# Kernel optimization log

Hardware: AMD Instinct MI355X
Metric: run time of the kernel (lower is better)

Reference implementation:

```python
import jax, jax.numpy as jnp
import numpy as np

EMBED_DIM = 256
NUM_HEADS = 8
PROJ_DIM = EMBED_DIM // NUM_HEADS


def setup_inputs() -> dict:
    key = jax.random.key(0)
    ks = jax.random.split(key, 5)
    scale = 1.0 / np.sqrt(EMBED_DIM)
    inputs = jax.random.normal(ks[0], (2, 12, 12, 12, EMBED_DIM), dtype=jnp.float32)
    Wq = jax.random.normal(ks[1], (EMBED_DIM, EMBED_DIM), dtype=jnp.float32) * scale
    Wk = jax.random.normal(ks[2], (EMBED_DIM, EMBED_DIM), dtype=jnp.float32) * scale
    Wv = jax.random.normal(ks[3], (EMBED_DIM, EMBED_DIM), dtype=jnp.float32) * scale
    Wo = jax.random.normal(ks[4], (EMBED_DIM, EMBED_DIM), dtype=jnp.float32) * scale
    z = jnp.zeros((EMBED_DIM,), dtype=jnp.float32)
    return {"inputs": inputs, "Wq": Wq, "bq": z, "Wk": Wk, "bk": z,
            "Wv": Wv, "bv": z, "Wo": Wo, "bo": z}


def reference(inputs, Wq, bq, Wk, bk, Wv, bv, Wo, bo):
    B, h, w, d, E = inputs.shape
    S = h * w * d  # flattened spatial sequence
    x = inputs.reshape(B, S, E)
    # projections + head split: [B, S, E] -> [B, H, S, P]
    def split_heads(t):
        return t.reshape(B, S, NUM_HEADS, PROJ_DIM).transpose(0, 2, 1, 3)
    q = split_heads(x @ Wq + bq)
    k = split_heads(x @ Wk + bk)
    v = split_heads(x @ Wv + bv)
    # NOTE: original module does NOT scale by 1/sqrt(proj_dim)
    scores = jnp.einsum('bhsp,bhtp->bhst', q, k)  # [B, H, S, S]
    attn = jax.nn.softmax(scores, axis=-1)
    out = jnp.einsum('bhst,bhtp->bhsp', attn, v)  # [B, H, S, P]
    out = out.transpose(0, 2, 1, 3).reshape(B, h, w, d, E)
    return out @ Wo + bo
```

## Files before the change

kernel.cpp:

```cpp
#include <hip/hip_runtime.h>
#include <math.h>

#define EMBED 256
#define HEADS 8
#define PDIM  32
#define BATCH 2
#define SEQ   1728
#define NTOK  (BATCH*SEQ)
#define NE    (NTOK*EMBED)
#define LOG2E 1.44269504088896f

typedef __attribute__((ext_vector_type(8))) __bf16 bf16x8;
typedef __attribute__((ext_vector_type(4))) float  f32x4;
typedef unsigned short ushort_t;

static __device__ __forceinline__ unsigned short f2bf_rne(float f) {
    union { float f; unsigned u; } x; x.f = f;
    unsigned r = x.u + 0x7fffu + ((x.u >> 16) & 1u);
    return (unsigned short)(r >> 16);
}
static __device__ __forceinline__ float bf2f(unsigned short h) {
    union { unsigned u; float f; } x; x.u = ((unsigned)h) << 16;
    return x.f;
}

__global__ __launch_bounds__(256) void convert_x_kernel(
    const float* __restrict__ x, ushort_t* __restrict__ xhi, ushort_t* __restrict__ xlo)
{
    const int i = (blockIdx.x * 256 + threadIdx.x) * 4;
    const float4 v = *(const float4*)&x[i];
    ushort4 h, l;
    h.x = f2bf_rne(v.x); l.x = f2bf_rne(v.x - bf2f(h.x));
    h.y = f2bf_rne(v.y); l.y = f2bf_rne(v.y - bf2f(h.y));
    h.z = f2bf_rne(v.z); l.z = f2bf_rne(v.z - bf2f(h.z));
    h.w = f2bf_rne(v.w); l.w = f2bf_rne(v.w - bf2f(h.w));
    *(ushort4*)&xhi[i] = h;
    *(ushort4*)&xlo[i] = l;
}

__global__ __launch_bounds__(256) void convert_w_kernel(
    const float* __restrict__ Wq, const float* __restrict__ Wk,
    const float* __restrict__ Wv, const float* __restrict__ Wo,
    ushort_t* __restrict__ wthi, ushort_t* __restrict__ wtlo)
{
    const int mat = blockIdx.z;
    const float* __restrict__ W = (mat == 0) ? Wq : (mat == 1) ? Wk : (mat == 2) ? Wv : Wo;
    const int k0 = blockIdx.x * 64, n0 = blockIdx.y * 64;
    const int t = threadIdx.x;

    __shared__ float Ws[64][68];
    {
        const int rr = t >> 4, cc = (t & 15) << 2;
        #pragma unroll
        for (int rep = 0; rep < 4; ++rep) {
            const int row = rr + rep * 16;
            *(float4*)&Ws[row][cc] = *(const float4*)&W[(size_t)(k0 + row) * EMBED + n0 + cc];
        }
    }
    __syncthreads();

    const int nl = t & 63;
    const int kc = (t >> 6) << 4;
    ushort_t hv[16], lv[16];
    #pragma unroll
    for (int kk = 0; kk < 16; ++kk) {
        const float v = Ws[kc + kk][nl];
        hv[kk] = f2bf_rne(v);
        lv[kk] = f2bf_rne(v - bf2f(hv[kk]));
    }
    ushort_t* dh = wthi + (size_t)mat * 65536 + (size_t)(n0 + nl) * EMBED + k0 + kc;
    ushort_t* dl = wtlo + (size_t)mat * 65536 + (size_t)(n0 + nl) * EMBED + k0 + kc;
    #pragma unroll
    for (int c = 0; c < 4; ++c) {
        *(ushort4*)&dh[c * 4] = *(ushort4*)&hv[c * 4];
        *(ushort4*)&dl[c * 4] = *(ushort4*)&lv[c * 4];
    }
}

__global__ __launch_bounds__(64) void qkv_gemm_kernel(
    const ushort_t* __restrict__ xhi, const ushort_t* __restrict__ xlo,
    const ushort_t* __restrict__ wthi, const ushort_t* __restrict__ wtlo,
    const float* __restrict__ bq, const float* __restrict__ bk, const float* __restrict__ bv,
    ushort_t* __restrict__ qo, ushort_t* __restrict__ ko, ushort_t* __restrict__ vt)
{
    const int lane = threadIdx.x, li = lane & 15, quad = lane >> 4;
    const int m0 = blockIdx.x * 64, n0 = blockIdx.y * 32, z = blockIdx.z;

    const ushort_t* aph = xhi + (size_t)(m0 + li) * EMBED + quad * 8;
    const ushort_t* apl = xlo + (size_t)(m0 + li) * EMBED + quad * 8;
    const ushort_t* bph = wthi + (size_t)z * 65536 + (size_t)(n0 + li) * EMBED + quad * 8;
    const ushort_t* bpl = wtlo + (size_t)z * 65536 + (size_t)(n0 + li) * EMBED + quad * 8;

    f32x4 acc[4][2];
    #pragma unroll
    for (int mt = 0; mt < 4; ++mt)
        #pragma unroll
        for (int nt = 0; nt < 2; ++nt)
            acc[mt][nt] = (f32x4){0.f, 0.f, 0.f, 0.f};

    #pragma unroll 2
    for (int k0 = 0; k0 < EMBED; k0 += 32) {
        bf16x8 ah[4], al[4], bh[2], bl[2];
        #pragma unroll
        for (int mt = 0; mt < 4; ++mt) {
            ah[mt] = *(const bf16x8*)(aph + (size_t)mt * 16 * EMBED + k0);
            al[mt] = *(const bf16x8*)(apl + (size_t)mt * 16 * EMBED + k0);
        }
        #pragma unroll
        for (int nt = 0; nt < 2; ++nt) {
            bh[nt] = *(const bf16x8*)(bph + (size_t)nt * 16 * EMBED + k0);
            bl[nt] = *(const bf16x8*)(bpl + (size_t)nt * 16 * EMBED + k0);
        }
        #pragma unroll
        for (int mt = 0; mt < 4; ++mt)
            #pragma unroll
            for (int nt = 0; nt < 2; ++nt) {
                acc[mt][nt] = __builtin_amdgcn_mfma_f32_16x16x32_bf16(ah[mt], bh[nt], acc[mt][nt], 0, 0, 0);
                acc[mt][nt] = __builtin_amdgcn_mfma_f32_16x16x32_bf16(al[mt], bh[nt], acc[mt][nt], 0, 0, 0);
                acc[mt][nt] = __builtin_amdgcn_mfma_f32_16x16x32_bf16(ah[mt], bl[nt], acc[mt][nt], 0, 0, 0);
            }
    }

    const int b = m0 / SEQ;
    const int sbase = m0 - b * SEQ;

    if (z <= 1) {
        ushort_t* __restrict__ dst = z ? ko : qo;
        const float* __restrict__ bias = z ? bk : bq;
        #pragma unroll
        for (int nt = 0; nt < 2; ++nt) {
            const int gcol = n0 + nt * 16 + li;
            const int h = gcol >> 5, p = gcol & 31;
            const float bb = bias[gcol];
            ushort_t* base = dst + ((size_t)(b * HEADS + h) * SEQ) * PDIM + p;
            #pragma unroll
            for (int mt = 0; mt < 4; ++mt)
                #pragma unroll
                for (int r = 0; r < 4; ++r) {
                    const int s = sbase + mt * 16 + quad * 4 + r;
                    base[(size_t)s * PDIM] = f2bf_rne(acc[mt][nt][r] + bb);
                }
        }
    } else {
        #pragma unroll
        for (int nt = 0; nt < 2; ++nt) {
            const int gcol = n0 + nt * 16 + li;
            const int h = gcol >> 5, p = gcol & 31;
            const float bb = bv[gcol];
            ushort_t* base = vt + ((size_t)(b * HEADS + h) * PDIM + p) * SEQ;
            #pragma unroll
            for (int mt = 0; mt < 4; ++mt) {
                const int s0 = sbase + mt * 16 + quad * 4;
                ushort4 w;
                w.x = f2bf_rne(acc[mt][nt][0] + bb);
                w.y = f2bf_rne(acc[mt][nt][1] + bb);
                w.z = f2bf_rne(acc[mt][nt][2] + bb);
                w.w = f2bf_rne(acc[mt][nt][3] + bb);
                *(ushort4*)&base[s0] = w;
            }
        }
    }
}

__global__ __launch_bounds__(64) void attn_kernel(
    const ushort_t* __restrict__ q, const ushort_t* __restrict__ k,
    const ushort_t* __restrict__ vt, ushort_t* __restrict__ aob)
{
    const int lane = threadIdx.x;
    const int li   = lane & 15;
    const int quad = lane >> 4;
    const int bh = blockIdx.y;
    const int b  = bh >> 3, h = bh & 7;
    const int q0 = blockIdx.x * 16;

    const ushort_t* __restrict__ qb = q  + (size_t)bh * SEQ * PDIM;
    const ushort_t* __restrict__ kb = k  + (size_t)bh * SEQ * PDIM;
    const ushort_t* __restrict__ vb = vt + (size_t)bh * PDIM * SEQ;

    __shared__ ushort_t Ps[16][72];

    const bf16x8 qfrag = *(const bf16x8*)(qb + (size_t)(q0 + li) * PDIM + quad * 8);

    const ushort_t* kptr = kb + (size_t)li * PDIM + quad * 8;
    const ushort_t* vptr = vb + (size_t)li * SEQ + quad * 8;

    f32x4 o0 = {0.f, 0.f, 0.f, 0.f};
    f32x4 o1 = {0.f, 0.f, 0.f, 0.f};
    float m_run = -__builtin_inff(), l_run = 0.f;

    bf16x8 kf0[4], vf0[4], kf1[4], vf1[4];

#define LOAD_TILE(KF, VF, J0) do {                                           \
        const ushort_t* kp = kptr + (size_t)(J0) * PDIM;                     \
        KF[0] = *(const bf16x8*)(kp);                                        \
        KF[1] = *(const bf16x8*)(kp + 16 * PDIM);                            \
        KF[2] = *(const bf16x8*)(kp + 32 * PDIM);                            \
        KF[3] = *(const bf16x8*)(kp + 48 * PDIM);                            \
        const ushort_t* vp = vptr + (J0);                                    \
        VF[0] = *(const bf16x8*)(vp);                                        \
        VF[1] = *(const bf16x8*)(vp + 16 * SEQ);                             \
        VF[2] = *(const bf16x8*)(vp + 32);                                   \
        VF[3] = *(const bf16x8*)(vp + 32 + 16 * SEQ);                        \
    } while (0)

    auto compute_tile = [&](const bf16x8* kf, const bf16x8* vf) {
        const f32x4 zero = {0.f, 0.f, 0.f, 0.f};
        f32x4 st[4];
        #pragma unroll
        for (int jt = 0; jt < 4; ++jt)
            st[jt] = __builtin_amdgcn_mfma_f32_16x16x32_bf16(kf[jt], qfrag, zero, 0, 0, 0);

        float tm = st[0][0];
        #pragma unroll
        for (int jt = 0; jt < 4; ++jt)
            #pragma unroll
            for (int r = 0; r < 4; ++r) tm = fmaxf(tm, st[jt][r]);
        tm = fmaxf(tm, __shfl_xor(tm, 16));
        tm = fmaxf(tm, __shfl_xor(tm, 32));
        const float mnew  = fmaxf(m_run, tm);
        const float negml = -(mnew * LOG2E);

        float ps = 0.f;
        #pragma unroll
        for (int jt = 0; jt < 4; ++jt) {
            const float p0 = __builtin_amdgcn_exp2f(fmaf(st[jt][0], LOG2E, negml));
            const float p1 = __builtin_amdgcn_exp2f(fmaf(st[jt][1], LOG2E, negml));
            const float p2 = __builtin_amdgcn_exp2f(fmaf(st[jt][2], LOG2E, negml));
            const float p3 = __builtin_amdgcn_exp2f(fmaf(st[jt][3], LOG2E, negml));
            ps += (p0 + p1) + (p2 + p3);
            uint2 pw;
            pw.x = __builtin_amdgcn_perm(__float_as_uint(p1) + 0x8000u,
                                         __float_as_uint(p0) + 0x8000u, 0x07060302u);
            pw.y = __builtin_amdgcn_perm(__float_as_uint(p3) + 0x8000u,
                                         __float_as_uint(p2) + 0x8000u, 0x07060302u);
            *(uint2*)&Ps[li][16 * jt + 4 * quad] = pw;
        }
        ps += __shfl_xor(ps, 16);
        ps += __shfl_xor(ps, 32);

        const float alpha = __builtin_amdgcn_exp2f(fmaf(m_run, LOG2E, negml));
        l_run = fmaf(l_run, alpha, ps);
        m_run = mnew;

        float af[4];
        #pragma unroll
        for (int r = 0; r < 4; ++r) af[r] = __shfl(alpha, 4 * quad + r);
        #pragma unroll
        for (int r = 0; r < 4; ++r) { o0[r] *= af[r]; o1[r] *= af[r]; }

        const bf16x8 pa0 = *(const bf16x8*)&Ps[li][8 * quad];
        const bf16x8 pa1 = *(const bf16x8*)&Ps[li][32 + 8 * quad];
        o0 = __builtin_amdgcn_mfma_f32_16x16x32_bf16(pa0, vf[0], o0, 0, 0, 0);
        o0 = __builtin_amdgcn_mfma_f32_16x16x32_bf16(pa1, vf[2], o0, 0, 0, 0);
        o1 = __builtin_amdgcn_mfma_f32_16x16x32_bf16(pa0, vf[1], o1, 0, 0, 0);
        o1 = __builtin_amdgcn_mfma_f32_16x16x32_bf16(pa1, vf[3], o1, 0, 0, 0);
    };

    LOAD_TILE(kf0, vf0, 0);
    for (int kt = 0; kt < SEQ / 64; kt += 2) {
        if (kt + 1 < SEQ / 64) LOAD_TILE(kf1, vf1, (kt + 1) * 64);
        compute_tile(kf0, vf0);
        if (kt + 1 < SEQ / 64) {
            if (kt + 2 < SEQ / 64) LOAD_TILE(kf0, vf0, (kt + 2) * 64);
            compute_tile(kf1, vf1);
        }
    }
#undef LOAD_TILE

    float linv[4];
    #pragma unroll
    for (int r = 0; r < 4; ++r) linv[r] = 1.0f / __shfl(l_run, 4 * quad + r);
    #pragma unroll
    for (int r = 0; r < 4; ++r) {
        const int s = q0 + 4 * quad + r;
        ushort_t* row = aob + ((size_t)(b * SEQ + s)) * EMBED + h * PDIM;
        row[li]      = f2bf_rne(o0[r] * linv[r]);
        row[16 + li] = f2bf_rne(o1[r] * linv[r]);
    }
}

__global__ __launch_bounds__(64) void out_gemm_kernel(
    const ushort_t* __restrict__ a, const ushort_t* __restrict__ wto,
    const float* __restrict__ bo, float* __restrict__ out)
{
    const int lane = threadIdx.x, li = lane & 15, quad = lane >> 4;
    const int m0 = blockIdx.x * 64, n0 = blockIdx.y * 16;

    const ushort_t* aph = a + (size_t)(m0 + li) * EMBED + quad * 8;
    const ushort_t* bph = wto + (size_t)(n0 + li) * EMBED + quad * 8;

    f32x4 acc[4];
    #pragma unroll
    for (int mt = 0; mt < 4; ++mt) acc[mt] = (f32x4){0.f, 0.f, 0.f, 0.f};

    #pragma unroll 2
    for (int k0 = 0; k0 < EMBED; k0 += 32) {
        bf16x8 ah[4];
        #pragma unroll
        for (int mt = 0; mt < 4; ++mt)
            ah[mt] = *(const bf16x8*)(aph + (size_t)mt * 16 * EMBED + k0);
        const bf16x8 bh = *(const bf16x8*)(bph + k0);
        #pragma unroll
        for (int mt = 0; mt < 4; ++mt)
            acc[mt] = __builtin_amdgcn_mfma_f32_16x16x32_bf16(ah[mt], bh, acc[mt], 0, 0, 0);
    }

    const int gcol = n0 + li;
    const float bb = bo[gcol];
    #pragma unroll
    for (int mt = 0; mt < 4; ++mt)
        #pragma unroll
        for (int r = 0; r < 4; ++r) {
            const int row = m0 + mt * 16 + quad * 4 + r;
            out[(size_t)row * EMBED + gcol] = acc[mt][r] + bb;
        }
}

extern "C" void kernel_launch(void* const* d_in, const int* in_sizes, int n_in,
                              void* d_out, int out_size, void* d_ws, size_t ws_size,
                              hipStream_t stream)
{
    const float* x  = (const float*)d_in[0];
    const float* Wq = (const float*)d_in[1];
    const float* bq = (const float*)d_in[2];
    const float* Wk = (const float*)d_in[3];
    const float* bk = (const float*)d_in[4];
    const float* Wv = (const float*)d_in[5];
    const float* bv = (const float*)d_in[6];
    const float* Wo = (const float*)d_in[7];
    const float* bo = (const float*)d_in[8];
    float* out = (float*)d_out;

    ushort_t* ws   = (ushort_t*)d_ws;
    ushort_t* xhi  = ws;
    ushort_t* xlo  = xhi + (size_t)NE;
    ushort_t* wthi = xlo + (size_t)NE;
    ushort_t* wtlo = wthi + 4 * 65536;
    ushort_t* qb   = wtlo + 4 * 65536;
    ushort_t* kb   = qb + (size_t)NE;
    ushort_t* vt   = kb + (size_t)NE;
    ushort_t* aob  = vt + (size_t)NE;

    convert_x_kernel<<<dim3(NE / 1024), 256, 0, stream>>>(x, xhi, xlo);
    convert_w_kernel<<<dim3(4, 4, 4), 256, 0, stream>>>(Wq, Wk, Wv, Wo, wthi, wtlo);
    qkv_gemm_kernel<<<dim3(NTOK / 64, 8, 3), 64, 0, stream>>>(
        xhi, xlo, wthi, wtlo, bq, bk, bv, qb, kb, vt);
    attn_kernel<<<dim3(SEQ / 16, BATCH * HEADS), 64, 0, stream>>>(qb, kb, vt, aob);
    out_gemm_kernel<<<dim3(NTOK / 64, 16), 64, 0, stream>>>(
        aob, wthi + 3 * 65536, bo, out);
}
```

Baseline: 137.6 us.

## Fuse fp32-to-bf16 conversion into GEMMs and split attention KV across warps

Measured after the change: 136.5 us. About the same (-0.8%).

```diff
diff --git a/kernel.cpp b/kernel.cpp
--- a/kernel.cpp
+++ b/kernel.cpp
@@ -13,112 +13,75 @@
 typedef __attribute__((ext_vector_type(8))) __bf16 bf16x8;
 typedef __attribute__((ext_vector_type(4))) float  f32x4;
 typedef unsigned short ushort_t;
+typedef unsigned int   uint_t;
 
 static __device__ __forceinline__ unsigned short f2bf_rne(float f) {
     union { float f; unsigned u; } x; x.f = f;
     unsigned r = x.u + 0x7fffu + ((x.u >> 16) & 1u);
     return (unsigned short)(r >> 16);
 }
-static __device__ __forceinline__ float bf2f(unsigned short h) {
-    union { unsigned u; float f; } x; x.u = ((unsigned)h) << 16;
-    return x.f;
-}
-
-__global__ __launch_bounds__(256) void convert_x_kernel(
-    const float* __restrict__ x, ushort_t* __restrict__ xhi, ushort_t* __restrict__ xlo)
-{
-    const int i = (blockIdx.x * 256 + threadIdx.x) * 4;
-    const float4 v = *(const float4*)&x[i];
-    ushort4 h, l;
-    h.x = f2bf_rne(v.x); l.x = f2bf_rne(v.x - bf2f(h.x));
-    h.y = f2bf_rne(v.y); l.y = f2bf_rne(v.y - bf2f(h.y));
-    h.z = f2bf_rne(v.z); l.z = f2bf_rne(v.z - bf2f(h.z));
-    h.w = f2bf_rne(v.w); l.w = f2bf_rne(v.w - bf2f(h.w));
-    *(ushort4*)&xhi[i] = h;
-    *(ushort4*)&xlo[i] = l;
-}
-
-__global__ __launch_bounds__(256) void convert_w_kernel(
-    const float* __restrict__ Wq, const float* __restrict__ Wk,
-    const float* __restrict__ Wv, const float* __restrict__ Wo,
-    ushort_t* __restrict__ wthi, ushort_t* __restrict__ wtlo)
-{
-    const int mat = blockIdx.z;
-    const float* __restrict__ W = (mat == 0) ? Wq : (mat == 1) ? Wk : (mat == 2) ? Wv : Wo;
-    const int k0 = blockIdx.x * 64, n0 = blockIdx.y * 64;
-    const int t = threadIdx.x;
-
-    __shared__ float Ws[64][68];
-    {
-        const int rr = t >> 4, cc = (t & 15) << 2;
-        #pragma unroll
-        for (int rep = 0; rep < 4; ++rep) {
-            const int row = rr + rep * 16;
-            *(float4*)&Ws[row][cc] = *(const float4*)&W[(size_t)(k0 + row) * EMBED + n0 + cc];
-        }
-    }
-    __syncthreads();
-
-    const int nl = t & 63;
-    const int kc = (t >> 6) << 4;
-    ushort_t hv[16], lv[16];
+union v8cast { uint4 u; bf16x8 v; };
+
+static __device__ __forceinline__ void cvt8_hilo(const float f[8], bf16x8& hi, bf16x8& lo) {
+    uint4 ph, pl;
+    uint_t* phv = (uint_t*)&ph; uint_t* plv = (uint_t*)&pl;
     #pragma unroll
-    for (int kk = 0; kk < 16; ++kk) {
-        const float v = Ws[kc + kk][nl];
-        hv[kk] = f2bf_rne(v);
-        lv[kk] = f2bf_rne(v - bf2f(hv[kk]));
-    }
-    ushort_t* dh = wthi + (size_t)mat * 65536 + (size_t)(n0 + nl) * EMBED + k0 + kc;
-    ushort_t* dl = wtlo + (size_t)mat * 65536 + (size_t)(n0 + nl) * EMBED + k0 + kc;
-    #pragma unroll
-    for (int c = 0; c < 4; ++c) {
-        *(ushort4*)&dh[c * 4] = *(ushort4*)&hv[c * 4];
-        *(ushort4*)&dl[c * 4] = *(ushort4*)&lv[c * 4];
-    }
+    for (int j = 0; j < 4; ++j) {
+        const float f0 = f[2 * j], f1 = f[2 * j + 1];
+        const uint_t u0 = __float_as_uint(f0) + 0x8000u;
+        const uint_t u1 = __float_as_uint(f1) + 0x8000u;
+        phv[j] = __builtin_amdgcn_perm(u1, u0, 0x07060302u);
+        const float l0 = f0 - __uint_as_float(u0 & 0xFFFF0000u);
+        const float l1 = f1 - __uint_as_float(u1 & 0xFFFF0000u);
+        plv[j] = __builtin_amdgcn_perm(__float_as_uint(l1) + 0x8000u,
+                                       __float_as_uint(l0) + 0x8000u, 0x07060302u);
+    }
+    v8cast ch; ch.u = ph; hi = ch.v;
+    v8cast cl; cl.u = pl; lo = cl.v;
 }
 
 __global__ __launch_bounds__(64) void qkv_gemm_kernel(
-    const ushort_t* __restrict__ xhi, const ushort_t* __restrict__ xlo,
-    const ushort_t* __restrict__ wthi, const ushort_t* __restrict__ wtlo,
-    const float* __restrict__ bq, const float* __restrict__ bk, const float* __restrict__ bv,
+    const float* __restrict__ x,
+    const float* __restrict__ Wq, const float* __restrict__ bq,
+    const float* __restrict__ Wk, const float* __restrict__ bk,
+    const float* __restrict__ Wv, const float* __restrict__ bv,
     ushort_t* __restrict__ qo, ushort_t* __restrict__ ko, ushort_t* __restrict__ vt)
 {
     const int lane = threadIdx.x, li = lane & 15, quad = lane >> 4;
-    const int m0 = blockIdx.x * 64, n0 = blockIdx.y * 32, z = blockIdx.z;
-
-    const ushort_t* aph = xhi + (size_t)(m0 + li) * EMBED + quad * 8;
-    const ushort_t* apl = xlo + (size_t)(m0 + li) * EMBED + quad * 8;
-    const ushort_t* bph = wthi + (size_t)z * 65536 + (size_t)(n0 + li) * EMBED + quad * 8;
-    const ushort_t* bpl = wtlo + (size_t)z * 65536 + (size_t)(n0 + li) * EMBED + quad * 8;
-
-    f32x4 acc[4][2];
+    const int m0 = blockIdx.x * 16, n0 = blockIdx.y * 32, z = blockIdx.z;
+    const float* __restrict__ W    = (z == 0) ? Wq : (z == 1) ? Wk : Wv;
+    const float* __restrict__ bias = (z == 0) ? bq : (z == 1) ? bk : bv;
+
+    const float* ap = x + (size_t)(m0 + li) * EMBED + quad * 8;
+
+    f32x4 acc[2];
+    acc[0] = (f32x4){0.f, 0.f, 0.f, 0.f};
+    acc[1] = (f32x4){0.f, 0.f, 0.f, 0.f};
+
     #pragma unroll
-    for (int mt = 0; mt < 4; ++mt)
-        #pragma unroll
-        for (int nt = 0; nt < 2; ++nt)
-            acc[mt][nt] = (f32x4){0.f, 0.f, 0.f, 0.f};
-
-    #pragma unroll 2
     for (int k0 = 0; k0 < EMBED; k0 += 32) {
-        bf16x8 ah[4], al[4], bh[2], bl[2];
-        #pragma unroll
-        for (int mt = 0; mt < 4; ++mt) {
-            ah[mt] = *(const bf16x8*)(aph + (size_t)mt * 16 * EMBED + k0);
-            al[mt] = *(const bf16x8*)(apl + (size_t)mt * 16 * EMBED + k0);
-        }
+        float af[8];
+        *(float4*)&af[0] = *(const float4*)(ap + k0);
+        *(float4*)&af[4] = *(const float4*)(ap + k0 + 4);
+        bf16x8 ah, al;
+        cvt8_hilo(af, ah, al);
+
+        bf16x8 bh[2], bl[2];
         #pragma unroll
         for (int nt = 0; nt < 2; ++nt) {
-            bh[nt] = *(const bf16x8*)(bph + (size_t)nt * 16 * EMBED + k0);
-            bl[nt] = *(const bf16x8*)(bpl + (size_t)nt * 16 * EMBED + k0);
-        }
-        #pragma unroll
-        for (int mt = 0; mt < 4; ++mt)
+            const int n = n0 + nt * 16 + li;
+            const float* wp = W + (size_t)(k0 + quad * 8) * EMBED + n;
+            float bf[8];
             #pragma unroll
-            for (int nt = 0; nt < 2; ++nt) {
-                acc[mt][nt] = __builtin_amdgcn_mfma_f32_16x16x32_bf16(ah[mt], bh[nt], acc[mt][nt], 0, 0, 0);
-                acc[mt][nt] = __builtin_amdgcn_mfma_f32_16x16x32_bf16(al[mt], bh[nt], acc[mt][nt], 0, 0, 0);
-                acc[mt][nt] = __builtin_amdgcn_mfma_f32_16x16x32_bf16(ah[mt], bl[nt], acc[mt][nt], 0, 0, 0);
-            }
+            for (int jj = 0; jj < 8; ++jj) bf[jj] = wp[(size_t)jj * EMBED];
+            cvt8_hilo(bf, bh[nt], bl[nt]);
+        }
+        #pragma unroll
+        for (int nt = 0; nt < 2; ++nt) {
+            acc[nt] = __builtin_amdgcn_mfma_f32_16x16x32_bf16(ah, bh[nt], acc[nt], 0, 0, 0);
+            acc[nt] = __builtin_amdgcn_mfma_f32_16x16x32_bf16(al, bh[nt], acc[nt], 0, 0, 0);
+            acc[nt] = __builtin_amdgcn_mfma_f32_16x16x32_bf16(ah, bl[nt], acc[nt], 0, 0, 0);
+        }
     }
 
     const int b = m0 / SEQ;
@@ -126,7 +89,6 @@
 
     if (z <= 1) {
         ushort_t* __restrict__ dst = z ? ko : qo;
-        const float* __restrict__ bias = z ? bk : bq;
         #pragma unroll
         for (int nt = 0; nt < 2; ++nt) {
             const int gcol = n0 + nt * 16 + li;
@@ -134,50 +96,51 @@
             const float bb = bias[gcol];
             ushort_t* base = dst + ((size_t)(b * HEADS + h) * SEQ) * PDIM + p;
             #pragma unroll
-            for (int mt = 0; mt < 4; ++mt)
-                #pragma unroll
-                for (int r = 0; r < 4; ++r) {
-                    const int s = sbase + mt * 16 + quad * 4 + r;
-                    base[(size_t)s * PDIM] = f2bf_rne(acc[mt][nt][r] + bb);
-                }
+            for (int r = 0; r < 4; ++r) {
+                const int s = sbase + quad * 4 + r;
+                base[(size_t)s * PDIM] = f2bf_rne(acc[nt][r] + bb);
+            }
         }
     } else {
         #pragma unroll
         for (int nt = 0; nt < 2; ++nt) {
             const int gcol = n0 + nt * 16 + li;
             const int h = gcol >> 5, p = gcol & 31;
-            const float bb = bv[gcol];
+            const float bb = bias[gcol];
             ushort_t* base = vt + ((size_t)(b * HEADS + h) * PDIM + p) * SEQ;
-            #pragma unroll
-            for (int mt = 0; mt < 4; ++mt) {
-                const int s0 = sbase + mt * 16 + quad * 4;
-                ushort4 w;
-                w.x = f2bf_rne(acc[mt][nt][0] + bb);
-                w.y = f2bf_rne(acc[mt][nt][1] + bb);
-                w.z = f2bf_rne(acc[mt][nt][2] + bb);
-                w.w = f2bf_rne(acc[mt][nt][3] + bb);
-                *(ushort4*)&base[s0] = w;
-            }
-        }
-    }
-}
-
-__global__ __launch_bounds__(64) void attn_kernel(
+            const int s0 = sbase + quad * 4;
+            ushort4 w;
+            w.x = f2bf_rne(acc[nt][0] + bb);
+            w.y = f2bf_rne(acc[nt][1] + bb);
+            w.z = f2bf_rne(acc[nt][2] + bb);
+            w.w = f2bf_rne(acc[nt][3] + bb);
+            *(ushort4*)&base[s0] = w;
+        }
+    }
+}
+
+__global__ __launch_bounds__(256) void attn_kernel(
     const ushort_t* __restrict__ q, const ushort_t* __restrict__ k,
     const ushort_t* __restrict__ vt, ushort_t* __restrict__ aob)
 {
-    const int lane = threadIdx.x;
+    const int t    = threadIdx.x;
+    const int lane = t & 63;
     const int li   = lane & 15;
     const int quad = lane >> 4;
+    const int w    = t >> 6;
+    const int pr   = w >> 1;
+    const int c    = w & 1;
     const int bh = blockIdx.y;
     const int b  = bh >> 3, h = bh & 7;
-    const int q0 = blockIdx.x * 16;
+    const int q0 = (blockIdx.x * 2 + pr) * 16;
 
     const ushort_t* __restrict__ qb = q  + (size_t)bh * SEQ * PDIM;
     const ushort_t* __restrict__ kb = k  + (size_t)bh * SEQ * PDIM;
     const ushort_t* __restrict__ vb = vt + (size_t)bh * PDIM * SEQ;
 
-    __shared__ ushort_t Ps[16][72];
+    __shared__ ushort_t Ps[4][16][72];
+    __shared__ float OS[2][16][32];
+    __shared__ float mS[2][16], lS[2][16];
 
     const bf16x8 qfrag = *(const bf16x8*)(qb + (size_t)(q0 + li) * PDIM + quad * 8);
 
@@ -233,7 +196,7 @@
                                          __float_as_uint(p0) + 0x8000u, 0x07060302u);
             pw.y = __builtin_amdgcn_perm(__float_as_uint(p3) + 0x8000u,
                                          __float_as_uint(p2) + 0x8000u, 0x07060302u);
-            *(uint2*)&Ps[li][16 * jt + 4 * quad] = pw;
+            *(uint2*)&Ps[w][li][16 * jt + 4 * quad] = pw;
         }
         ps += __shfl_xor(ps, 16);
         ps += __shfl_xor(ps, 32);
@@ -248,72 +211,92 @@
         #pragma unroll
         for (int r = 0; r < 4; ++r) { o0[r] *= af[r]; o1[r] *= af[r]; }
 
-        const bf16x8 pa0 = *(const bf16x8*)&Ps[li][8 * quad];
-        const bf16x8 pa1 = *(const bf16x8*)&Ps[li][32 + 8 * quad];
+        const bf16x8 pa0 = *(const bf16x8*)&Ps[w][li][8 * quad];
+        const bf16x8 pa1 = *(const bf16x8*)&Ps[w][li][32 + 8 * quad];
         o0 = __builtin_amdgcn_mfma_f32_16x16x32_bf16(pa0, vf[0], o0, 0, 0, 0);
         o0 = __builtin_amdgcn_mfma_f32_16x16x32_bf16(pa1, vf[2], o0, 0, 0, 0);
         o1 = __builtin_amdgcn_mfma_f32_16x16x32_bf16(pa0, vf[1], o1, 0, 0, 0);
         o1 = __builtin_amdgcn_mfma_f32_16x16x32_bf16(pa1, vf[3], o1, 0, 0, 0);
     };
 
-    LOAD_TILE(kf0, vf0, 0);
-    for (int kt = 0; kt < SEQ / 64; kt += 2) {
-        if (kt + 1 < SEQ / 64) LOAD_TILE(kf1, vf1, (kt + 1) * 64);
+    const int jstart = c ? 896 : 0;
+    const int ntl    = c ? 13 : 14;
+
+    LOAD_TILE(kf0, vf0, jstart);
+    for (int kt = 0; kt < ntl; kt += 2) {
+        if (kt + 1 < ntl) LOAD_TILE(kf1, vf1, jstart + (kt + 1) * 64);
         compute_tile(kf0, vf0);
-        if (kt + 1 < SEQ / 64) {
-            if (kt + 2 < SEQ / 64) LOAD_TILE(kf0, vf0, (kt + 2) * 64);
+        if (kt + 1 < ntl) {
+            if (kt + 2 < ntl) LOAD_TILE(kf0, vf0, jstart + (kt + 2) * 64);
             compute_tile(kf1, vf1);
         }
     }
 #undef LOAD_TILE
 
-    float linv[4];
-    #pragma unroll
-    for (int r = 0; r < 4; ++r) linv[r] = 1.0f / __shfl(l_run, 4 * quad + r);
-    #pragma unroll
-    for (int r = 0; r < 4; ++r) {
-        const int s = q0 + 4 * quad + r;
-        ushort_t* row = aob + ((size_t)(b * SEQ + s)) * EMBED + h * PDIM;
-        row[li]      = f2bf_rne(o0[r] * linv[r]);
-        row[16 + li] = f2bf_rne(o1[r] * linv[r]);
+    if (c == 1) {
+        if (quad == 0) { mS[pr][li] = m_run; lS[pr][li] = l_run; }
+        #pragma unroll
+        for (int r = 0; r < 4; ++r) {
+            OS[pr][4 * quad + r][li]      = o0[r];
+            OS[pr][4 * quad + r][16 + li] = o1[r];
+        }
+    }
+    __syncthreads();
+    if (c == 0) {
+        const float m1 = mS[pr][li], l1 = lS[pr][li];
+        const float M  = fmaxf(m_run, m1);
+        const float a0 = __builtin_amdgcn_exp2f((m_run - M) * LOG2E);
+        const float a1 = __builtin_amdgcn_exp2f((m1    - M) * LOG2E);
+        const float lt = a0 * l_run + a1 * l1;
+        #pragma unroll
+        for (int r = 0; r < 4; ++r) {
+            const int row = 4 * quad + r;
+            const float af0  = __shfl(a0, row);
+            const float af1  = __shfl(a1, row);
+            const float linv = 1.0f / __shfl(lt, row);
+            const float v0 = (af0 * o0[r] + af1 * OS[pr][row][li])      * linv;
+            const float v1 = (af0 * o1[r] + af1 * OS[pr][row][16 + li]) * linv;
+            const int s = q0 + row;
+            ushort_t* orow = aob + ((size_t)(b * SEQ + s)) * EMBED + h * PDIM;
+            orow[li]      = f2bf_rne(v0);
+            orow[16 + li] = f2bf_rne(v1);
+        }
     }
 }
 
 __global__ __launch_bounds__(64) void out_gemm_kernel(
-    const ushort_t* __restrict__ a, const ushort_t* __restrict__ wto,
+    const ushort_t* __restrict__ a, const float* __restrict__ Wo,
     const float* __restrict__ bo, float* __restrict__ out)
 {
     const int lane = threadIdx.x, li = lane & 15, quad = lane >> 4;
-    const int m0 = blockIdx.x * 64, n0 = blockIdx.y * 16;
+    const int m0 = blockIdx.x * 16, n0 = blockIdx.y * 16;
 
     const ushort_t* aph = a + (size_t)(m0 + li) * EMBED + quad * 8;
-    const ushort_t* bph = wto + (size_t)(n0 + li) * EMBED + quad * 8;
-
-    f32x4 acc[4];
+
+    f32x4 acc = {0.f, 0.f, 0.f, 0.f};
+
     #pragma unroll
-    for (int mt = 0; mt < 4; ++mt) acc[mt] = (f32x4){0.f, 0.f, 0.f, 0.f};
-
-    #pragma unroll 2
     for (int k0 = 0; k0 < EMBED; k0 += 32) {
-        bf16x8 ah[4];
-        #pragma unroll
-        for (int mt = 0; mt < 4; ++mt)
-            ah[mt] = *(const bf16x8*)(aph + (size_t)mt * 16 * EMBED + k0);
-        const bf16x8 bh = *(const bf16x8*)(bph + k0);
-        #pragma unroll
-        for (int mt = 0; mt < 4; ++mt)
-            acc[mt] = __builtin_amdgcn_mfma_f32_16x16x32_bf16(ah[mt], bh, acc[mt], 0, 0, 0);
-    }
-
-    const int gcol = n0 + li;
-    const float bb = bo[gcol];
+        const bf16x8 ah = *(const bf16x8*)(aph + k0);
+        const float* wp = Wo + (size_t)(k0 + quad * 8) * EMBED + n0 + li;
+        uint4 pb;
+        uint_t* pbv = (uint_t*)&pb;
+        #pragma unroll
+        for (int j = 0; j < 4; ++j) {
+            const uint_t u0 = __float_as_uint(wp[(size_t)(2 * j) * EMBED])     + 0x8000u;
+            const uint_t u1 = __float_as_uint(wp[(size_t)(2 * j + 1) * EMBED]) + 0x8000u;
+            pbv[j] = __builtin_amdgcn_perm(u1, u0, 0x07060302u);
+        }
+        v8cast cb; cb.u = pb;
+        acc = __builtin_amdgcn_mfma_f32_16x16x32_bf16(ah, cb.v, acc, 0, 0, 0);
+    }
+
+    const float bb = bo[n0 + li];
     #pragma unroll
-    for (int mt = 0; mt < 4; ++mt)
-        #pragma unroll
-        for (int r = 0; r < 4; ++r) {
-            const int row = m0 + mt * 16 + quad * 4 + r;
-            out[(size_t)row * EMBED + gcol] = acc[mt][r] + bb;
-        }
+    for (int r = 0; r < 4; ++r) {
+        const int row = m0 + 4 * quad + r;
+        out[(size_t)row * EMBED + n0 + li] = acc[r] + bb;
+    }
 }
 
 extern "C" void kernel_launch(void* const* d_in, const int* in_sizes, int n_in,
@@ -331,21 +314,14 @@
     const float* bo = (const float*)d_in[8];
     float* out = (float*)d_out;
 
-    ushort_t* ws   = (ushort_t*)d_ws;
-    ushort_t* xhi  = ws;
-    ushort_t* xlo  = xhi + (size_t)NE;
-    ushort_t* wthi = xlo + (size_t)NE;
-    ushort_t* wtlo = wthi + 4 * 65536;
-    ushort_t* qb   = wtlo + 4 * 65536;
-    ushort_t* kb   = qb + (size_t)NE;
-    ushort_t* vt   = kb + (size_t)NE;
-    ushort_t* aob  = vt + (size_t)NE;
-
-    convert_x_kernel<<<dim3(NE / 1024), 256, 0, stream>>>(x, xhi, xlo);
-    convert_w_kernel<<<dim3(4, 4, 4), 256, 0, stream>>>(Wq, Wk, Wv, Wo, wthi, wtlo);
-    qkv_gemm_kernel<<<dim3(NTOK / 64, 8, 3), 64, 0, stream>>>(
-        xhi, xlo, wthi, wtlo, bq, bk, bv, qb, kb, vt);
-    attn_kernel<<<dim3(SEQ / 16, BATCH * HEADS), 64, 0, stream>>>(qb, kb, vt, aob);
-    out_gemm_kernel<<<dim3(NTOK / 64, 16), 64, 0, stream>>>(
-        aob, wthi + 3 * 65536, bo, out);
-}
+    ushort_t* ws  = (ushort_t*)d_ws;
+    ushort_t* qb  = ws;
+    ushort_t* kb  = qb + (size_t)NE;
+    ushort_t* vt  = kb + (size_t)NE;
+    ushort_t* aob = vt + (size_t)NE;
+
+    qkv_gemm_kernel<<<dim3(NTOK / 16, 8, 3), 64, 0, stream>>>(
+        x, Wq, bq, Wk, bk, Wv, bv, qb, kb, vt);
+    attn_kernel<<<dim3(SEQ / 32, BATCH * HEADS), 256, 0, stream>>>(qb, kb, vt, aob);
+    out_gemm_kernel<<<dim3(NTOK / 16, 16), 64, 0, stream>>>(aob, Wo, bo, out);
+}
```
